# Kernel tuning notes

Hardware: AMD Instinct MI355X
Metric: run time of the kernel (lower is better)

Reference implementation:

```python
import jax, jax.numpy as jnp
import numpy as np

N_T, N_I = 4096, 4096
TEXT_DIM, IMAGE_DIM, HIDDEN_DIM = 1024, 1024, 1024


def setup_inputs() -> dict:
    key = jax.random.key(0)
    ks = jax.random.split(key, 8)
    s_t = 1.0 / np.sqrt(TEXT_DIM)
    s_i = 1.0 / np.sqrt(IMAGE_DIM)
    return {
        "text_features": jax.random.normal(ks[0], (N_T, TEXT_DIM), jnp.float32),
        "image_features": jax.random.normal(ks[1], (N_I, IMAGE_DIM), jnp.float32),
        # nn.Linear params: weight [out, in], bias [out]
        "w_text": jax.random.uniform(ks[2], (HIDDEN_DIM, TEXT_DIM), jnp.float32, -s_t, s_t),
        "b_text": jax.random.uniform(ks[3], (HIDDEN_DIM,), jnp.float32, -s_t, s_t),
        "w_image": jax.random.uniform(ks[4], (HIDDEN_DIM, IMAGE_DIM), jnp.float32, -s_i, s_i),
        "b_image": jax.random.uniform(ks[5], (HIDDEN_DIM,), jnp.float32, -s_i, s_i),
        "scale_TI": jnp.ones((1,), jnp.float32),
        "scale_IT": jnp.ones((1,), jnp.float32),
    }


def reference(text_features, image_features, w_text, b_text, w_image, b_image, scale_TI, scale_IT):
    # linear projections to shared hidden space
    t = text_features @ w_text.T + b_text      # [N_t, H]
    i = image_features @ w_image.T + b_image   # [N_i, H]
    inv_sqrt_h = 1.0 / jnp.sqrt(jnp.asarray(HIDDEN_DIM, t.dtype))
    # text -> image attention: softmax over image axis, scaled post-softmax
    logits_TI = (t @ i.T) * inv_sqrt_h               # [N_t, N_i]
    attn_TI = jax.nn.softmax(logits_TI, axis=-1) * scale_TI
    # image -> text attention
    attn_IT = jax.nn.softmax(logits_TI.T, axis=-1) * scale_IT  # [N_i, N_t]
    text_attention_on_image = attn_TI @ image_features  # [N_t, image_dim]
    image_attention_on_text = attn_IT @ text_features   # [N_i, text_dim]
    return (text_attention_on_image, image_attention_on_text)
```

## Files before the change

kernel.cpp:

```cpp
#include <hip/hip_runtime.h>


typedef __bf16 bf16x8 __attribute__((ext_vector_type(8)));
typedef float f32x4 __attribute__((ext_vector_type(4)));

#define N_T 4096
#define N_I 4096
#define DIM 1024
#define TSS 136

#define AT_SLOT 24576
#define AT_LDS_BYTES (3 * AT_SLOT * 2)

__device__ __forceinline__ unsigned short f2bf(float f) {
    unsigned int u = __float_as_uint(f);
    u += 0x7fffu + ((u >> 16) & 1u);
    return (unsigned short)(u >> 16);
}

__device__ __forceinline__ void async_cp16(const unsigned short* g, unsigned short* l) {
    __builtin_amdgcn_global_load_lds(
        (const __attribute__((address_space(1))) unsigned int*)g,
        (__attribute__((address_space(3))) unsigned int*)l, 16, 0, 0);
}

__device__ __forceinline__ void stage_async(const unsigned short* __restrict__ src,
                                            int ld, int row0, int k0,
                                            unsigned short* lds, int t) {
    int r = t >> 2, c = (t & 3) << 3;
    const unsigned short* g = src + (size_t)(row0 + r) * ld + k0 + c;
    async_cp16(g, lds + r * 32 + c);
    async_cp16(g + (size_t)64 * ld, lds + (64 + r) * 32 + c);
}

__device__ __forceinline__ void stage_async64(const unsigned short* __restrict__ src,
                                              int ld, int row0, int k0,
                                              unsigned short* lds, int t) {
    int r = t >> 2, c = (t & 3) << 3;
    async_cp16(src + (size_t)(row0 + r) * ld + k0 + c, lds + r * 32 + c);
}

__device__ __forceinline__ void mfma_step(const unsigned short* As,
                                          const unsigned short* Bs, f32x4 acc[4][4],
                                          int wrow, int wcol, int lane16, int quad) {
    bf16x8 a[4], b[4];
#pragma unroll
    for (int i = 0; i < 4; ++i) {
        a[i] = *(const bf16x8*)&As[(wrow + i * 16 + lane16) * 32 + quad * 8];
        b[i] = *(const bf16x8*)&Bs[(wcol + i * 16 + lane16) * 32 + quad * 8];
    }
#pragma unroll
    for (int i = 0; i < 4; ++i)
#pragma unroll
        for (int j = 0; j < 4; ++j)
            acc[i][j] = __builtin_amdgcn_mfma_f32_16x16x32_bf16(a[i], b[j], acc[i][j], 0, 0, 0);
}

__device__ __forceinline__ void mfma_step42(const unsigned short* As,
                                            const unsigned short* Bs, f32x4 acc[4][2],
                                            int wrow, int wcol, int lane16, int quad) {
    bf16x8 a[4], b[2];
#pragma unroll
    for (int i = 0; i < 4; ++i)
        a[i] = *(const bf16x8*)&As[(wrow + i * 16 + lane16) * 32 + quad * 8];
#pragma unroll
    for (int j = 0; j < 2; ++j)
        b[j] = *(const bf16x8*)&Bs[(wcol + j * 16 + lane16) * 32 + quad * 8];
#pragma unroll
    for (int i = 0; i < 4; ++i)
#pragma unroll
        for (int j = 0; j < 2; ++j)
            acc[i][j] = __builtin_amdgcn_mfma_f32_16x16x32_bf16(a[i], b[j], acc[i][j], 0, 0, 0);
}

__device__ __forceinline__ void tile_store(const unsigned short* sm,
                                           unsigned short* __restrict__ g, int ld,
                                           int row0, int col0, int tid) {
    int r = tid >> 1, h = (tid & 1) << 6;
    const unsigned short* src = sm + r * TSS + h;
    unsigned short* dst = g + (size_t)(row0 + r) * ld + col0 + h;
#pragma unroll
    for (int v = 0; v < 8; ++v)
        *(uint4*)(dst + v * 8) = *(const uint4*)(src + v * 8);
}

__global__ void __launch_bounds__(256)
cvt_all(const float* __restrict__ im, const float* __restrict__ tx,
        const float* __restrict__ wt, const float* __restrict__ wi,
        unsigned short* __restrict__ imb, unsigned short* __restrict__ txb,
        unsigned short* __restrict__ imgT, unsigned short* __restrict__ textT,
        unsigned short* __restrict__ wtb, unsigned short* __restrict__ wib,
        float* __restrict__ lTI) {
    int t = threadIdx.x;
    if (blockIdx.z == 2) {
        int lin = blockIdx.y * 64 + blockIdx.x;
        if (lin < 4) {
            *(f32x4*)&lTI[(lin * 256 + t) * 8] = (f32x4){0.f, 0.f, 0.f, 0.f};
            *(f32x4*)&lTI[(lin * 256 + t) * 8 + 4] = (f32x4){0.f, 0.f, 0.f, 0.f};
        }
        size_t i = (size_t)(lin * 256 + t) * 8;
        const float* s;
        unsigned short* d;
        size_t off;
        if (i < 1048576) { s = wt; d = wtb; off = i; }
        else             { s = wi; d = wib; off = i - 1048576; }
        float4 f0 = *(const float4*)(s + off);
        float4 f1 = *(const float4*)(s + off + 4);
        uint4 o;
        o.x = (unsigned int)f2bf(f0.x) | ((unsigned int)f2bf(f0.y) << 16);
        o.y = (unsigned int)f2bf(f0.z) | ((unsigned int)f2bf(f0.w) << 16);
        o.z = (unsigned int)f2bf(f1.x) | ((unsigned int)f2bf(f1.y) << 16);
        o.w = (unsigned int)f2bf(f1.z) | ((unsigned int)f2bf(f1.w) << 16);
        *(uint4*)(d + off) = o;
        return;
    }
    const float* in = blockIdx.z ? tx : im;
    unsigned short* nb = blockIdx.z ? txb : imb;
    unsigned short* tr = blockIdx.z ? textT : imgT;
    __shared__ float tile[64][65];
    int row0 = blockIdx.x * 64, col0 = blockIdx.y * 64;
    int r = t >> 2, c = (t & 3) << 4;
    {
        const float* p = in + (size_t)(row0 + r) * DIM + col0 + c;
        float4 f0 = *(const float4*)(p);
        float4 f1 = *(const float4*)(p + 4);
        float4 f2 = *(const float4*)(p + 8);
        float4 f3 = *(const float4*)(p + 12);
        *(float4*)&tile[r][c] = f0;
        *(float4*)&tile[r][c + 4] = f1;
        *(float4*)&tile[r][c + 8] = f2;
        *(float4*)&tile[r][c + 12] = f3;
        uint4 o0, o1;
        o0.x = (unsigned int)f2bf(f0.x) | ((unsigned int)f2bf(f0.y) << 16);
        o0.y = (unsigned int)f2bf(f0.z) | ((unsigned int)f2bf(f0.w) << 16);
        o0.z = (unsigned int)f2bf(f1.x) | ((unsigned int)f2bf(f1.y) << 16);
        o0.w = (unsigned int)f2bf(f1.z) | ((unsigned int)f2bf(f1.w) << 16);
        o1.x = (unsigned int)f2bf(f2.x) | ((unsigned int)f2bf(f2.y) << 16);
        o1.y = (unsigned int)f2bf(f2.z) | ((unsigned int)f2bf(f2.w) << 16);
        o1.z = (unsigned int)f2bf(f3.x) | ((unsigned int)f2bf(f3.y) << 16);
        o1.w = (unsigned int)f2bf(f3.z) | ((unsigned int)f2bf(f3.w) << 16);
        unsigned short* q = nb + (size_t)(row0 + r) * DIM + col0 + c;
        *(uint4*)q = o0;
        *(uint4*)(q + 8) = o1;
    }
    __syncthreads();
    {
        unsigned short v[16];
#pragma unroll
        for (int u = 0; u < 16; ++u) v[u] = f2bf(tile[c + u][r]);
        unsigned short* q = tr + (size_t)(col0 + r) * N_T + row0 + c;
        *(uint4*)q = *(uint4*)&v[0];
        *(uint4*)(q + 8) = *(uint4*)&v[8];
    }
}

__global__ void __launch_bounds__(256, 4)
gemm_proj2(const unsigned short* __restrict__ Atx, const unsigned short* __restrict__ Wtx,
           const float* __restrict__ btx, unsigned short* __restrict__ Ctx,
           const unsigned short* __restrict__ Aim, const unsigned short* __restrict__ Wim,
           const float* __restrict__ bim, unsigned short* __restrict__ Cim) {
    __shared__ unsigned short As[2][128 * 32];
    __shared__ unsigned short Bs[2][64 * 32];
    int z = blockIdx.z;
    const unsigned short* A = z ? Aim : Atx;
    const unsigned short* W = z ? Wim : Wtx;
    const float* bias = z ? bim : btx;
    unsigned short* C = z ? Cim : Ctx;
    int tid = threadIdx.x;
    int m0 = blockIdx.x * 128, n0 = blockIdx.y * 64;
    int lane = tid & 63, wave = tid >> 6;
    int lane16 = lane & 15, quad = lane >> 4;
    int wrow = (wave >> 1) * 64, wcol = (wave & 1) * 32;
    f32x4 acc[4][2];
    {
        f32x4 zz = {0.f, 0.f, 0.f, 0.f};
        for (int i = 0; i < 4; ++i)
            for (int j = 0; j < 2; ++j) acc[i][j] = zz;
    }
    for (int k0 = 0; k0 < DIM; k0 += 64) {
        stage_async(A, DIM, m0, k0, As[0], tid);
        stage_async64(W, DIM, n0, k0, Bs[0], tid);
        stage_async(A, DIM, m0, k0 + 32, As[1], tid);
        stage_async64(W, DIM, n0, k0 + 32, Bs[1], tid);
        __syncthreads();
        mfma_step42(As[0], Bs[0], acc, wrow, wcol, lane16, quad);
        mfma_step42(As[1], Bs[1], acc, wrow, wcol, lane16, quad);
        __syncthreads();
    }
#pragma unroll
    for (int j = 0; j < 2; ++j) {
        int col = n0 + wcol + j * 16 + lane16;
        float bv = bias[col];
#pragma unroll
        for (int i = 0; i < 4; ++i) {
            int rowb = m0 + wrow + i * 16 + quad * 4;
#pragma unroll
            for (int r = 0; r < 4; ++r)
                C[(size_t)(rowb + r) * DIM + col] = f2bf(acc[i][j][r] + bv);
        }
    }
}

__global__ void __launch_bounds__(256, 4)
gemm_logits_exp(const unsigned short* __restrict__ Tb,
                const unsigned short* __restrict__ Ib,
                unsigned short* __restrict__ P, unsigned short* __restrict__ PT,
                float* __restrict__ lT, float* __restrict__ lI) {
    __shared__ unsigned short smem[128 * TSS];
    unsigned short* As0 = smem;
    unsigned short* Bs0 = smem + 4096;
    unsigned short* As1 = smem + 8192;
    unsigned short* Bs1 = smem + 12288;
    float* lred = (float*)(smem + 16384);
    float* cred = lred + 128;
    int tid = threadIdx.x;
    int m0 = blockIdx.x * 128, n0 = blockIdx.y * 128;
    int lane = tid & 63, wave = tid >> 6;
    int lane16 = lane & 15, quad = lane >> 4;
    int wrow = (wave >> 1) * 64, wcol = (wave & 1) * 64;
    f32x4 acc[4][4];
    {
        f32x4 z = {0.f, 0.f, 0.f, 0.f};
        for (int i = 0; i < 4; ++i)
            for (int j = 0; j < 4; ++j) acc[i][j] = z;
    }
    for (int k0 = 0; k0 < DIM; k0 += 64) {
        stage_async(Tb, DIM, m0, k0, As0, tid);
        stage_async(Ib, DIM, n0, k0, Bs0, tid);
        stage_async(Tb, DIM, m0, k0 + 32, As1, tid);
        stage_async(Ib, DIM, n0, k0 + 32, Bs1, tid);
        __syncthreads();
        mfma_step(As0, Bs0, acc, wrow, wcol, lane16, quad);
        mfma_step(As1, Bs1, acc, wrow, wcol, lane16, quad);
        __syncthreads();
    }
#pragma unroll
    for (int i = 0; i < 4; ++i)
#pragma unroll
        for (int j = 0; j < 4; ++j)
#pragma unroll
            for (int r = 0; r < 4; ++r)
                acc[i][j][r] = __expf(acc[i][j][r] * 0.03125f);
    float rs[4][4];
#pragma unroll
    for (int i = 0; i < 4; ++i)
#pragma unroll
        for (int r = 0; r < 4; ++r) {
            float s = acc[i][0][r] + acc[i][1][r] + acc[i][2][r] + acc[i][3][r];
            s += __shfl_xor(s, 1); s += __shfl_xor(s, 2);
            s += __shfl_xor(s, 4); s += __shfl_xor(s, 8);
            rs[i][r] = s;
        }
    float cs[4];
#pragma unroll
    for (int j = 0; j < 4; ++j) {
        float s = 0.f;
#pragma unroll
        for (int i = 0; i < 4; ++i)
#pragma unroll
            for (int r = 0; r < 4; ++r) s += acc[i][j][r];
        s += __shfl_xor(s, 16); s += __shfl_xor(s, 32);
        cs[j] = s;
    }
    if (wave & 1) {
        if (lane16 == 0)
#pragma unroll
            for (int i = 0; i < 4; ++i)
#pragma unroll
                for (int r = 0; r < 4; ++r)
                    lred[wrow + i * 16 + quad * 4 + r] = rs[i][r];
    }
    if (wave >> 1) {
        if (quad == 0)
#pragma unroll
            for (int j = 0; j < 4; ++j)
                cred[wcol + j * 16 + lane16] = cs[j];
    }
    __syncthreads();
    if (!(wave & 1) && lane16 == 0) {
#pragma unroll
        for (int i = 0; i < 4; ++i)
#pragma unroll
            for (int r = 0; r < 4; ++r) {
                int row = wrow + i * 16 + quad * 4 + r;
                atomicAdd(&lT[m0 + row], rs[i][r] + lred[row]);
            }
    }
    if (!(wave >> 1) && quad == 0) {
#pragma unroll
        for (int j = 0; j < 4; ++j) {
            int col = wcol + j * 16 + lane16;
            atomicAdd(&lI[n0 + col], cs[j] + cred[col]);
        }
    }
    __syncthreads();
#pragma unroll
    for (int i = 0; i < 4; ++i)
#pragma unroll
        for (int j = 0; j < 4; ++j)
#pragma unroll
            for (int r = 0; r < 4; ++r)
                smem[(wrow + i * 16 + quad * 4 + r) * TSS + wcol + j * 16 + lane16] =
                    f2bf(acc[i][j][r]);
    __syncthreads();
    tile_store(smem, P, N_I, m0, n0, tid);
    __syncthreads();
#pragma unroll
    for (int i = 0; i < 4; ++i)
#pragma unroll
        for (int j = 0; j < 4; ++j) {
            unsigned int lo = (unsigned int)f2bf(acc[i][j][0]) |
                              ((unsigned int)f2bf(acc[i][j][1]) << 16);
            unsigned int hi = (unsigned int)f2bf(acc[i][j][2]) |
                              ((unsigned int)f2bf(acc[i][j][3]) << 16);
            uint2 v; v.x = lo; v.y = hi;
            *(uint2*)&smem[(wcol + j * 16 + lane16) * TSS + wrow + i * 16 + quad * 4] = v;
        }
    __syncthreads();
    tile_store(smem, PT, N_T, n0, m0, tid);
}


__device__ __forceinline__ void at_stageA_half(const unsigned short* __restrict__ g,
                                               int row0, int k0, unsigned short* lds,
                                               int t, int h) {
#pragma unroll
    for (int u = 0; u < 2; ++u) {
        int c = t + (h * 2 + u) * 512;
        int r = c >> 3;
        int kq = (c & 7) ^ (r & 7);
        async_cp16(g + (size_t)(row0 + r) * 4096 + k0 + (kq << 3), lds + c * 8);
    }
}

__device__ __forceinline__ void at_stageB_half(const unsigned short* __restrict__ g,
                                               int row0, int k0, unsigned short* lds,
                                               int t, int h) {
    int c = t + h * 512;
    int r = c >> 3;
    int kq = (c & 7) ^ (r & 7);
    async_cp16(g + (size_t)(row0 + r) * 4096 + k0 + (kq << 3), lds + c * 8);
}

__device__ __forceinline__ void at_stageA(const unsigned short* __restrict__ g,
                                          int row0, int k0, unsigned short* lds, int t) {
    at_stageA_half(g, row0, k0, lds, t, 0);
    at_stageA_half(g, row0, k0, lds, t, 1);
}
__device__ __forceinline__ void at_stageB(const unsigned short* __restrict__ g,
                                          int row0, int k0, unsigned short* lds, int t) {
    at_stageB_half(g, row0, k0, lds, t, 0);
    at_stageB_half(g, row0, k0, lds, t, 1);
}

template <int DO_STAGE>
__device__ __forceinline__ void at_sub(const unsigned short* cp,
                                       const unsigned short* __restrict__ A,
                                       const unsigned short* __restrict__ Bt,
                                       int m0, int n0, int kst, unsigned short* nsl,
                                       int t, f32x4 acc[4][4],
                                       int wrow, int wcol, int lane16, int quad, int ks) {
    const unsigned short* As = cp;
    const unsigned short* Bs = cp + 16384;
    bf16x8 a[4], b[4];
    int sw = (((ks << 2) | quad) ^ (lane16 & 7)) << 3;
#pragma unroll
    for (int i = 0; i < 4; ++i)
        a[i] = *(const bf16x8*)&As[(wrow + i * 16 + lane16) * 64 + sw];
#pragma unroll
    for (int j = 0; j < 4; ++j)
        b[j] = *(const bf16x8*)&Bs[(wcol + j * 16 + lane16) * 64 + sw];
    if (DO_STAGE) {
        at_stageA_half(A, m0, kst, nsl, t, ks);
        at_stageB_half(Bt, n0, kst, nsl + 16384, t, ks);
    }
    __builtin_amdgcn_s_setprio(1);
#pragma unroll
    for (int i = 0; i < 4; ++i)
#pragma unroll
        for (int j = 0; j < 4; ++j)
            acc[i][j] = __builtin_amdgcn_mfma_f32_16x16x32_bf16(a[i], b[j], acc[i][j], 0, 0, 0);
    __builtin_amdgcn_s_setprio(0);
}

__global__ void __launch_bounds__(512)
gemm_attn3(const unsigned short* __restrict__ P, const unsigned short* __restrict__ imgT,
           const float* __restrict__ lT, const float* __restrict__ sTI,
           float* __restrict__ out0,
           const unsigned short* __restrict__ PT, const unsigned short* __restrict__ textT,
           const float* __restrict__ lI, const float* __restrict__ sIT,
           float* __restrict__ out1) {
    extern __shared__ unsigned short sm[];
    int which = blockIdx.z;
    const unsigned short* A = which ? PT : P;
    const unsigned short* Bt = which ? textT : imgT;
    const float* l = which ? lI : lT;
    const float* sp = which ? sIT : sTI;
    float* out = which ? out1 : out0;

    int tid = threadIdx.x;
    int m0 = blockIdx.x * 256, n0 = blockIdx.y * 128;
    int lane = tid & 63, wave = tid >> 6;
    int lane16 = lane & 15, quad = lane >> 4;
    int wrow = (wave >> 1) * 64, wcol = (wave & 1) * 64;
    f32x4 acc[4][4];
    {
        f32x4 z = {0.f, 0.f, 0.f, 0.f};
        for (int i = 0; i < 4; ++i)
            for (int j = 0; j < 4; ++j) acc[i][j] = z;
    }

    at_stageA(A, m0, 0, sm, tid);
    at_stageB(Bt, n0, 0, sm + 16384, tid);
    at_stageA(A, m0, 64, sm + AT_SLOT, tid);
    at_stageB(Bt, n0, 64, sm + AT_SLOT + 16384, tid);
    asm volatile("s_waitcnt vmcnt(6)" ::: "memory");
    __builtin_amdgcn_s_barrier();

    int cur = 0;
    for (int s = 0; s < 62; ++s) {
        int ns = cur + 2; if (ns >= 3) ns -= 3;
        unsigned short* nsl = sm + ns * AT_SLOT;
        const unsigned short* cp = sm + cur * AT_SLOT;
        int kst = (s + 2) * 64;
        at_sub<1>(cp, A, Bt, m0, n0, kst, nsl, tid, acc, wrow, wcol, lane16, quad, 0);
        asm volatile("" ::: "memory");
        __builtin_amdgcn_s_barrier();
        asm volatile("" ::: "memory");
        at_sub<1>(cp, A, Bt, m0, n0, kst, nsl, tid, acc, wrow, wcol, lane16, quad, 1);
        asm volatile("s_waitcnt vmcnt(6) lgkmcnt(0)" ::: "memory");
        __builtin_amdgcn_s_barrier();
        cur += 1; if (cur >= 3) cur -= 3;
    }
    {
        const unsigned short* cp = sm + cur * AT_SLOT;
        at_sub<0>(cp, A, Bt, m0, n0, 0, nullptr, tid, acc, wrow, wcol, lane16, quad, 0);
        asm volatile("" ::: "memory");
        __builtin_amdgcn_s_barrier();
        asm volatile("" ::: "memory");
        at_sub<0>(cp, A, Bt, m0, n0, 0, nullptr, tid, acc, wrow, wcol, lane16, quad, 1);
        asm volatile("s_waitcnt vmcnt(0) lgkmcnt(0)" ::: "memory");
        __builtin_amdgcn_s_barrier();
        cur += 1; if (cur >= 3) cur -= 3;
    }
    {
        const unsigned short* cp = sm + cur * AT_SLOT;
        at_sub<0>(cp, A, Bt, m0, n0, 0, nullptr, tid, acc, wrow, wcol, lane16, quad, 0);
        at_sub<0>(cp, A, Bt, m0, n0, 0, nullptr, tid, acc, wrow, wcol, lane16, quad, 1);
    }

    float sc = sp[0];
#pragma unroll
    for (int i = 0; i < 4; ++i) {
        int rowb = m0 + wrow + i * 16 + quad * 4;
        float fac[4];
#pragma unroll
        for (int r = 0; r < 4; ++r) fac[r] = sc / l[rowb + r];
#pragma unroll
        for (int j = 0; j < 4; ++j) {
            int col = n0 + wcol + j * 16 + lane16;
#pragma unroll
            for (int r = 0; r < 4; ++r)
                out[(size_t)(rowb + r) * DIM + col] = acc[i][j][r] * fac[r];
        }
    }
}

extern "C" void kernel_launch(void* const* d_in, const int* in_sizes, int n_in,
                              void* d_out, int out_size, void* d_ws, size_t ws_size,
                              hipStream_t stream) {
    const float* text = (const float*)d_in[0];
    const float* image = (const float*)d_in[1];
    const float* w_text = (const float*)d_in[2];
    const float* b_text = (const float*)d_in[3];
    const float* w_image = (const float*)d_in[4];
    const float* b_image = (const float*)d_in[5];
    const float* scale_TI = (const float*)d_in[6];
    const float* scale_IT = (const float*)d_in[7];
    float* out0 = (float*)d_out;
    float* out1 = out0 + (size_t)N_T * DIM;

    char* ws = (char*)d_ws;
    unsigned short* text_bf = (unsigned short*)(ws);
    unsigned short* image_bf = (unsigned short*)(ws + (8ull << 20));
    unsigned short* wt_bf = (unsigned short*)(ws + (16ull << 20));
    unsigned short* wi_bf = (unsigned short*)(ws + (18ull << 20));
    unsigned short* P = (unsigned short*)(ws);
    unsigned short* imgT = (unsigned short*)(ws + (32ull << 20));
    unsigned short* textT = (unsigned short*)(ws + (40ull << 20));
    unsigned short* t_bf = (unsigned short*)(ws + (48ull << 20));
    unsigned short* i_bf = (unsigned short*)(ws + (56ull << 20));
    unsigned short* PT = (unsigned short*)(ws + (64ull << 20));
    float* lT = (float*)(ws + (96ull << 20));
    float* lI = (float*)(ws + (96ull << 20) + 16384);

    static bool lds_set = false;
    if (!lds_set) {
        hipFuncSetAttribute((const void*)gemm_attn3,
                            hipFuncAttributeMaxDynamicSharedMemorySize, AT_LDS_BYTES);
        lds_set = true;
    }

    cvt_all<<<dim3(N_T / 64, DIM / 64, 3), 256, 0, stream>>>(
        image, text, w_text, w_image, image_bf, text_bf, imgT, textT,
        wt_bf, wi_bf, lT);

    gemm_proj2<<<dim3(N_T / 128, DIM / 64, 2), 256, 0, stream>>>(
        text_bf, wt_bf, b_text, t_bf, image_bf, wi_bf, b_image, i_bf);

    gemm_logits_exp<<<dim3(N_T / 128, N_I / 128), 256, 0, stream>>>(t_bf, i_bf, P, PT, lT, lI);

    gemm_attn3<<<dim3(N_T / 256, DIM / 128, 2), 512, AT_LDS_BYTES, stream>>>(
        P, imgT, lT, scale_TI, out0, PT, textT, lI, scale_IT, out1);
}
```

Baseline: 246.1 us.

## Port logits GEMM to 256x128 tiles with triple-buffered swizzled async pipeline

The logits/exp GEMM now uses the same 512-thread, triple-buffered, XOR-swizzled async LDS pipeline as the attention GEMM, with a 256x128 tile in place of 128x128. Staging helpers are templated on leading dimension so both kernels can share them. The aim is to overlap global loads with MFMA work and reduce LDS bank conflicts and sync stalls. Column sums are now reduced across four wave bands, and the transposed tile store uses a wider padded layout. In exchange, dynamic LDS use grows and there are fewer blocks in flight.

```diff
diff --git a/kernel.cpp b/kernel.cpp
--- a/kernel.cpp
+++ b/kernel.cpp
@@ -8,6 +8,7 @@
 #define N_I 4096
 #define DIM 1024
 #define TSS 136
+#define PTS 264
 
 #define AT_SLOT 24576
 #define AT_LDS_BYTES (3 * AT_SLOT * 2)
@@ -40,22 +41,6 @@
     async_cp16(src + (size_t)(row0 + r) * ld + k0 + c, lds + r * 32 + c);
 }
 
-__device__ __forceinline__ void mfma_step(const unsigned short* As,
-                                          const unsigned short* Bs, f32x4 acc[4][4],
-                                          int wrow, int wcol, int lane16, int quad) {
-    bf16x8 a[4], b[4];
-#pragma unroll
-    for (int i = 0; i < 4; ++i) {
-        a[i] = *(const bf16x8*)&As[(wrow + i * 16 + lane16) * 32 + quad * 8];
-        b[i] = *(const bf16x8*)&Bs[(wcol + i * 16 + lane16) * 32 + quad * 8];
-    }
-#pragma unroll
-    for (int i = 0; i < 4; ++i)
-#pragma unroll
-        for (int j = 0; j < 4; ++j)
-            acc[i][j] = __builtin_amdgcn_mfma_f32_16x16x32_bf16(a[i], b[j], acc[i][j], 0, 0, 0);
-}
-
 __device__ __forceinline__ void mfma_step42(const unsigned short* As,
                                             const unsigned short* Bs, f32x4 acc[4][2],
                                             int wrow, int wcol, int lane16, int quad) {
@@ -73,11 +58,89 @@
             acc[i][j] = __builtin_amdgcn_mfma_f32_16x16x32_bf16(a[i], b[j], acc[i][j], 0, 0, 0);
 }
 
-__device__ __forceinline__ void tile_store(const unsigned short* sm,
-                                           unsigned short* __restrict__ g, int ld,
-                                           int row0, int col0, int tid) {
+
+template <int LD>
+__device__ __forceinline__ void at_stageA_half(const unsigned short* __restrict__ g,
+                                               int row0, int k0, unsigned short* lds,
+                                               int t, int h) {
+#pragma unroll
+    for (int u = 0; u < 2; ++u) {
+        int c = t + (h * 2 + u) * 512;
+        int r = c >> 3;
+        int kq = (c & 7) ^ (r & 7);
+        async_cp16(g + (size_t)(row0 + r) * LD + k0 + (kq << 3), lds + c * 8);
+    }
+}
+
+template <int LD>
+__device__ __forceinline__ void at_stageB_half(const unsigned short* __restrict__ g,
+                                               int row0, int k0, unsigned short* lds,
+                                               int t, int h) {
+    int c = t + h * 512;
+    int r = c >> 3;
+    int kq = (c & 7) ^ (r & 7);
+    async_cp16(g + (size_t)(row0 + r) * LD + k0 + (kq << 3), lds + c * 8);
+}
+
+template <int LD>
+__device__ __forceinline__ void at_stageA(const unsigned short* __restrict__ g,
+                                          int row0, int k0, unsigned short* lds, int t) {
+    at_stageA_half<LD>(g, row0, k0, lds, t, 0);
+    at_stageA_half<LD>(g, row0, k0, lds, t, 1);
+}
+template <int LD>
+__device__ __forceinline__ void at_stageB(const unsigned short* __restrict__ g,
+                                          int row0, int k0, unsigned short* lds, int t) {
+    at_stageB_half<LD>(g, row0, k0, lds, t, 0);
+    at_stageB_half<LD>(g, row0, k0, lds, t, 1);
+}
+
+template <int LD, int DO_STAGE>
+__device__ __forceinline__ void at_sub(const unsigned short* cp,
+                                       const unsigned short* __restrict__ A,
+                                       const unsigned short* __restrict__ Bt,
+                                       int m0, int n0, int kst, unsigned short* nsl,
+                                       int t, f32x4 acc[4][4],
+                                       int wrow, int wcol, int lane16, int quad, int ks) {
+    const unsigned short* As = cp;
+    const unsigned short* Bs = cp + 16384;
+    bf16x8 a[4], b[4];
+    int sw = (((ks << 2) | quad) ^ (lane16 & 7)) << 3;
+#pragma unroll
+    for (int i = 0; i < 4; ++i)
+        a[i] = *(const bf16x8*)&As[(wrow + i * 16 + lane16) * 64 + sw];
+#pragma unroll
+    for (int j = 0; j < 4; ++j)
+        b[j] = *(const bf16x8*)&Bs[(wcol + j * 16 + lane16) * 64 + sw];
+    if (DO_STAGE) {
+        at_stageA_half<LD>(A, m0, kst, nsl, t, ks);
+        at_stageB_half<LD>(Bt, n0, kst, nsl + 16384, t, ks);
+    }
+    __builtin_amdgcn_s_setprio(1);
+#pragma unroll
+    for (int i = 0; i < 4; ++i)
+#pragma unroll
+        for (int j = 0; j < 4; ++j)
+            acc[i][j] = __builtin_amdgcn_mfma_f32_16x16x32_bf16(a[i], b[j], acc[i][j], 0, 0, 0);
+    __builtin_amdgcn_s_setprio(0);
+}
+
+__device__ __forceinline__ void tile_store256(const unsigned short* smp,
+                                              unsigned short* __restrict__ g, int ld,
+                                              int row0, int col0, int tid) {
     int r = tid >> 1, h = (tid & 1) << 6;
-    const unsigned short* src = sm + r * TSS + h;
+    const unsigned short* src = smp + r * TSS + h;
+    unsigned short* dst = g + (size_t)(row0 + r) * ld + col0 + h;
+#pragma unroll
+    for (int v = 0; v < 8; ++v)
+        *(uint4*)(dst + v * 8) = *(const uint4*)(src + v * 8);
+}
+
+__device__ __forceinline__ void tile_store128x256(const unsigned short* smp,
+                                                  unsigned short* __restrict__ g, int ld,
+                                                  int row0, int col0, int tid) {
+    int r = tid >> 2, h = (tid & 3) << 6;
+    const unsigned short* src = smp + r * PTS + h;
     unsigned short* dst = g + (size_t)(row0 + r) * ld + col0 + h;
 #pragma unroll
     for (int v = 0; v < 8; ++v)
@@ -201,20 +264,14 @@
     }
 }
 
-__global__ void __launch_bounds__(256, 4)
+__global__ void __launch_bounds__(512)
 gemm_logits_exp(const unsigned short* __restrict__ Tb,
                 const unsigned short* __restrict__ Ib,
                 unsigned short* __restrict__ P, unsigned short* __restrict__ PT,
                 float* __restrict__ lT, float* __restrict__ lI) {
-    __shared__ unsigned short smem[128 * TSS];
-    unsigned short* As0 = smem;
-    unsigned short* Bs0 = smem + 4096;
-    unsigned short* As1 = smem + 8192;
-    unsigned short* Bs1 = smem + 12288;
-    float* lred = (float*)(smem + 16384);
-    float* cred = lred + 128;
+    extern __shared__ unsigned short sm[];
     int tid = threadIdx.x;
-    int m0 = blockIdx.x * 128, n0 = blockIdx.y * 128;
+    int m0 = blockIdx.x * 256, n0 = blockIdx.y * 128;
     int lane = tid & 63, wave = tid >> 6;
     int lane16 = lane & 15, quad = lane >> 4;
     int wrow = (wave >> 1) * 64, wcol = (wave & 1) * 64;
@@ -224,16 +281,46 @@
         for (int i = 0; i < 4; ++i)
             for (int j = 0; j < 4; ++j) acc[i][j] = z;
     }
-    for (int k0 = 0; k0 < DIM; k0 += 64) {
-        stage_async(Tb, DIM, m0, k0, As0, tid);
-        stage_async(Ib, DIM, n0, k0, Bs0, tid);
-        stage_async(Tb, DIM, m0, k0 + 32, As1, tid);
-        stage_async(Ib, DIM, n0, k0 + 32, Bs1, tid);
-        __syncthreads();
-        mfma_step(As0, Bs0, acc, wrow, wcol, lane16, quad);
-        mfma_step(As1, Bs1, acc, wrow, wcol, lane16, quad);
-        __syncthreads();
-    }
+
+    at_stageA<DIM>(Tb, m0, 0, sm, tid);
+    at_stageB<DIM>(Ib, n0, 0, sm + 16384, tid);
+    at_stageA<DIM>(Tb, m0, 64, sm + AT_SLOT, tid);
+    at_stageB<DIM>(Ib, n0, 64, sm + AT_SLOT + 16384, tid);
+    asm volatile("s_waitcnt vmcnt(6)" ::: "memory");
+    __builtin_amdgcn_s_barrier();
+
+    int cur = 0;
+    for (int s = 0; s < 14; ++s) {
+        int ns = cur + 2; if (ns >= 3) ns -= 3;
+        unsigned short* nsl = sm + ns * AT_SLOT;
+        const unsigned short* cp = sm + cur * AT_SLOT;
+        int kst = (s + 2) * 64;
+        at_sub<DIM, 1>(cp, Tb, Ib, m0, n0, kst, nsl, tid, acc, wrow, wcol, lane16, quad, 0);
+        asm volatile("" ::: "memory");
+        __builtin_amdgcn_s_barrier();
+        asm volatile("" ::: "memory");
+        at_sub<DIM, 1>(cp, Tb, Ib, m0, n0, kst, nsl, tid, acc, wrow, wcol, lane16, quad, 1);
+        asm volatile("s_waitcnt vmcnt(6) lgkmcnt(0)" ::: "memory");
+        __builtin_amdgcn_s_barrier();
+        cur += 1; if (cur >= 3) cur -= 3;
+    }
+    {
+        const unsigned short* cp = sm + cur * AT_SLOT;
+        at_sub<DIM, 0>(cp, Tb, Ib, m0, n0, 0, nullptr, tid, acc, wrow, wcol, lane16, quad, 0);
+        asm volatile("" ::: "memory");
+        __builtin_amdgcn_s_barrier();
+        asm volatile("" ::: "memory");
+        at_sub<DIM, 0>(cp, Tb, Ib, m0, n0, 0, nullptr, tid, acc, wrow, wcol, lane16, quad, 1);
+        asm volatile("s_waitcnt vmcnt(0) lgkmcnt(0)" ::: "memory");
+        __builtin_amdgcn_s_barrier();
+        cur += 1; if (cur >= 3) cur -= 3;
+    }
+    {
+        const unsigned short* cp = sm + cur * AT_SLOT;
+        at_sub<DIM, 0>(cp, Tb, Ib, m0, n0, 0, nullptr, tid, acc, wrow, wcol, lane16, quad, 0);
+        at_sub<DIM, 0>(cp, Tb, Ib, m0, n0, 0, nullptr, tid, acc, wrow, wcol, lane16, quad, 1);
+    }
+
 #pragma unroll
     for (int i = 0; i < 4; ++i)
 #pragma unroll
@@ -262,6 +349,10 @@
         s += __shfl_xor(s, 16); s += __shfl_xor(s, 32);
         cs[j] = s;
     }
+    float* lred = (float*)(sm + 35840);
+    float* cred = lred + 256;
+    int band = wave >> 1;
+    __syncthreads();
     if (wave & 1) {
         if (lane16 == 0)
 #pragma unroll
@@ -270,12 +361,20 @@
                 for (int r = 0; r < 4; ++r)
                     lred[wrow + i * 16 + quad * 4 + r] = rs[i][r];
     }
-    if (wave >> 1) {
+    if (band) {
         if (quad == 0)
 #pragma unroll
             for (int j = 0; j < 4; ++j)
-                cred[wcol + j * 16 + lane16] = cs[j];
-    }
+                cred[(band - 1) * 128 + wcol + j * 16 + lane16] = cs[j];
+    }
+#pragma unroll
+    for (int i = 0; i < 4; ++i)
+#pragma unroll
+        for (int j = 0; j < 4; ++j)
+#pragma unroll
+            for (int r = 0; r < 4; ++r)
+                sm[(wrow + i * 16 + quad * 4 + r) * TSS + wcol + j * 16 + lane16] =
+                    f2bf(acc[i][j][r]);
     __syncthreads();
     if (!(wave & 1) && lane16 == 0) {
 #pragma unroll
@@ -286,24 +385,14 @@
                 atomicAdd(&lT[m0 + row], rs[i][r] + lred[row]);
             }
     }
-    if (!(wave >> 1) && quad == 0) {
+    if (!band && quad == 0) {
 #pragma unroll
         for (int j = 0; j < 4; ++j) {
-            int col = wcol + j * 16 + lane16;
-            atomicAdd(&lI[n0 + col], cs[j] + cred[col]);
+            int c = wcol + j * 16 + lane16;
+            atomicAdd(&lI[n0 + c], cs[j] + cred[c] + cred[128 + c] + cred[256 + c]);
         }
     }
-    __syncthreads();
-#pragma unroll
-    for (int i = 0; i < 4; ++i)
-#pragma unroll
-        for (int j = 0; j < 4; ++j)
-#pragma unroll
-            for (int r = 0; r < 4; ++r)
-                smem[(wrow + i * 16 + quad * 4 + r) * TSS + wcol + j * 16 + lane16] =
-                    f2bf(acc[i][j][r]);
-    __syncthreads();
-    tile_store(smem, P, N_I, m0, n0, tid);
+    tile_store256(sm, P, N_I, m0, n0, tid);
     __syncthreads();
 #pragma unroll
     for (int i = 0; i < 4; ++i)
@@ -314,73 +403,10 @@
             unsigned int hi = (unsigned int)f2bf(acc[i][j][2]) |
                               ((unsigned int)f2bf(acc[i][j][3]) << 16);
             uint2 v; v.x = lo; v.y = hi;
-            *(uint2*)&smem[(wcol + j * 16 + lane16) * TSS + wrow + i * 16 + quad * 4] = v;
+            *(uint2*)&sm[(wcol + j * 16 + lane16) * PTS + wrow + i * 16 + quad * 4] = v;
         }
     __syncthreads();
-    tile_store(smem, PT, N_T, n0, m0, tid);
-}
-
-
-__device__ __forceinline__ void at_stageA_half(const unsigned short* __restrict__ g,
-                                               int row0, int k0, unsigned short* lds,
-                                               int t, int h) {
-#pragma unroll
-    for (int u = 0; u < 2; ++u) {
-        int c = t + (h * 2 + u) * 512;
-        int r = c >> 3;
-        int kq = (c & 7) ^ (r & 7);
-        async_cp16(g + (size_t)(row0 + r) * 4096 + k0 + (kq << 3), lds + c * 8);
-    }
-}
-
-__device__ __forceinline__ void at_stageB_half(const unsigned short* __restrict__ g,
-                                               int row0, int k0, unsigned short* lds,
-                                               int t, int h) {
-    int c = t + h * 512;
-    int r = c >> 3;
-    int kq = (c & 7) ^ (r & 7);
-    async_cp16(g + (size_t)(row0 + r) * 4096 + k0 + (kq << 3), lds + c * 8);
-}
-
-__device__ __forceinline__ void at_stageA(const unsigned short* __restrict__ g,
-                                          int row0, int k0, unsigned short* lds, int t) {
-    at_stageA_half(g, row0, k0, lds, t, 0);
-    at_stageA_half(g, row0, k0, lds, t, 1);
-}
-__device__ __forceinline__ void at_stageB(const unsigned short* __restrict__ g,
-                                          int row0, int k0, unsigned short* lds, int t) {
-    at_stageB_half(g, row0, k0, lds, t, 0);
-    at_stageB_half(g, row0, k0, lds, t, 1);
-}
-
-template <int DO_STAGE>
-__device__ __forceinline__ void at_sub(const unsigned short* cp,
-                                       const unsigned short* __restrict__ A,
-                                       const unsigned short* __restrict__ Bt,
-                                       int m0, int n0, int kst, unsigned short* nsl,
-                                       int t, f32x4 acc[4][4],
-                                       int wrow, int wcol, int lane16, int quad, int ks) {
-    const unsigned short* As = cp;
-    const unsigned short* Bs = cp + 16384;
-    bf16x8 a[4], b[4];
-    int sw = (((ks << 2) | quad) ^ (lane16 & 7)) << 3;
-#pragma unroll
-    for (int i = 0; i < 4; ++i)
-        a[i] = *(const bf16x8*)&As[(wrow + i * 16 + lane16) * 64 + sw];
-#pragma unroll
-    for (int j = 0; j < 4; ++j)
-        b[j] = *(const bf16x8*)&Bs[(wcol + j * 16 + lane16) * 64 + sw];
-    if (DO_STAGE) {
-        at_stageA_half(A, m0, kst, nsl, t, ks);
-        at_stageB_half(Bt, n0, kst, nsl + 16384, t, ks);
-    }
-    __builtin_amdgcn_s_setprio(1);
-#pragma unroll
-    for (int i = 0; i < 4; ++i)
-#pragma unroll
-        for (int j = 0; j < 4; ++j)
-            acc[i][j] = __builtin_amdgcn_mfma_f32_16x16x32_bf16(a[i], b[j], acc[i][j], 0, 0, 0);
-    __builtin_amdgcn_s_setprio(0);
+    tile_store128x256(sm, PT, N_T, n0, m0, tid);
 }
 
 __global__ void __launch_bounds__(512)
@@ -410,10 +436,10 @@
             for (int j = 0; j < 4; ++j) acc[i][j] = z;
     }
 
-    at_stageA(A, m0, 0, sm, tid);
-    at_stageB(Bt, n0, 0, sm + 16384, tid);
-    at_stageA(A, m0, 64, sm + AT_SLOT, tid);
-    at_stageB(Bt, n0, 64, sm + AT_SLOT + 16384, tid);
+    at_stageA<4096>(A, m0, 0, sm, tid);
+    at_stageB<4096>(Bt, n0, 0, sm + 16384, tid);
+    at_stageA<4096>(A, m0, 64, sm + AT_SLOT, tid);
+    at_stageB<4096>(Bt, n0, 64, sm + AT_SLOT + 16384, tid);
     asm volatile("s_waitcnt vmcnt(6)" ::: "memory");
     __builtin_amdgcn_s_barrier();
 
@@ -423,30 +449,30 @@
         unsigned short* nsl = sm + ns * AT_SLOT;
         const unsigned short* cp = sm + cur * AT_SLOT;
         int kst = (s + 2) * 64;
-        at_sub<1>(cp, A, Bt, m0, n0, kst, nsl, tid, acc, wrow, wcol, lane16, quad, 0);
-        asm volatile("" ::: "memory");
-        __builtin_amdgcn_s_barrier();
-        asm volatile("" ::: "memory");
-        at_sub<1>(cp, A, Bt, m0, n0, kst, nsl, tid, acc, wrow, wcol, lane16, quad, 1);
+        at_sub<4096, 1>(cp, A, Bt, m0, n0, kst, nsl, tid, acc, wrow, wcol, lane16, quad, 0);
+        asm volatile("" ::: "memory");
+        __builtin_amdgcn_s_barrier();
+        asm volatile("" ::: "memory");
+        at_sub<4096, 1>(cp, A, Bt, m0, n0, kst, nsl, tid, acc, wrow, wcol, lane16, quad, 1);
         asm volatile("s_waitcnt vmcnt(6) lgkmcnt(0)" ::: "memory");
         __builtin_amdgcn_s_barrier();
         cur += 1; if (cur >= 3) cur -= 3;
     }
     {
         const unsigned short* cp = sm + cur * AT_SLOT;
-        at_sub<0>(cp, A, Bt, m0, n0, 0, nullptr, tid, acc, wrow, wcol, lane16, quad, 0);
-        asm volatile("" ::: "memory");
-        __builtin_amdgcn_s_barrier();
-        asm volatile("" ::: "memory");
-        at_sub<0>(cp, A, Bt, m0, n0, 0, nullptr, tid, acc, wrow, wcol, lane16, quad, 1);
+        at_sub<4096, 0>(cp, A, Bt, m0, n0, 0, nullptr, tid, acc, wrow, wcol, lane16, quad, 0);
+        asm volatile("" ::: "memory");
+        __builtin_amdgcn_s_barrier();
+        asm volatile("" ::: "memory");
+        at_sub<4096, 0>(cp, A, Bt, m0, n0, 0, nullptr, tid, acc, wrow, wcol, lane16, quad, 1);
         asm volatile("s_waitcnt vmcnt(0) lgkmcnt(0)" ::: "memory");
         __builtin_amdgcn_s_barrier();
         cur += 1; if (cur >= 3) cur -= 3;
     }
     {
         const unsigned short* cp = sm + cur * AT_SLOT;
-        at_sub<0>(cp, A, Bt, m0, n0, 0, nullptr, tid, acc, wrow, wcol, lane16, quad, 0);
-        at_sub<0>(cp, A, Bt, m0, n0, 0, nullptr, tid, acc, wrow, wcol, lane16, quad, 1);
+        at_sub<4096, 0>(cp, A, Bt, m0, n0, 0, nullptr, tid, acc, wrow, wcol, lane16, quad, 0);
+        at_sub<4096, 0>(cp, A, Bt, m0, n0, 0, nullptr, tid, acc, wrow, wcol, lane16, quad, 1);
     }
 
     float sc = sp[0];
@@ -498,6 +524,8 @@
     if (!lds_set) {
         hipFuncSetAttribute((const void*)gemm_attn3,
                             hipFuncAttributeMaxDynamicSharedMemorySize, AT_LDS_BYTES);
+        hipFuncSetAttribute((const void*)gemm_logits_exp,
+                            hipFuncAttributeMaxDynamicSharedMemorySize, AT_LDS_BYTES);
         lds_set = true;
     }
 
@@ -508,7 +536,8 @@
     gemm_proj2<<<dim3(N_T / 128, DIM / 64, 2), 256, 0, stream>>>(
         text_bf, wt_bf, b_text, t_bf, image_bf, wi_bf, b_image, i_bf);
 
-    gemm_logits_exp<<<dim3(N_T / 128, N_I / 128), 256, 0, stream>>>(t_bf, i_bf, P, PT, lT, lI);
+    gemm_logits_exp<<<dim3(N_T / 256, N_I / 128), 512, AT_LDS_BYTES, stream>>>(
+        t_bf, i_bf, P, PT, lT, lI);
 
     gemm_attn3<<<dim3(N_T / 256, DIM / 128, 2), 512, AT_LDS_BYTES, stream>>>(
         P, imgT, lT, scale_TI, out0, PT, textT, lI, scale_IT, out1);
```

Result: slower. 252.5 us (+2.6%).

## Load A fragments directly from global into registers, stage only B in LDS

Applied to the files above, without the earlier changes.

The attention GEMM stops staging the A operand (the softmax probability matrix) through LDS. Each wave now loads its A fragments straight from global memory into registers, double-buffered one k-tile ahead, while B keeps the 3-slot async LDS pipeline. This cuts LDS footprint from 144KB to 48KB, which may allow more blocks per CU, and removes the LDS write and read traffic for A. The cost is that A rows are no longer shared between the two waves with the same wrow, so global and L2 load traffic for A doubles. It also needs more registers and exposes global load latency directly to the MFMA loop.

```diff
diff --git a/kernel.cpp b/kernel.cpp
--- a/kernel.cpp
+++ b/kernel.cpp
@@ -9,8 +9,7 @@
 #define DIM 1024
 #define TSS 136
 
-#define AT_SLOT 24576
-#define AT_LDS_BYTES (3 * AT_SLOT * 2)
+#define BT_SLOT 8192
 
 __device__ __forceinline__ unsigned short f2bf(float f) {
     unsigned int u = __float_as_uint(f);
@@ -321,18 +320,6 @@
 }
 
 
-__device__ __forceinline__ void at_stageA_half(const unsigned short* __restrict__ g,
-                                               int row0, int k0, unsigned short* lds,
-                                               int t, int h) {
-#pragma unroll
-    for (int u = 0; u < 2; ++u) {
-        int c = t + (h * 2 + u) * 512;
-        int r = c >> 3;
-        int kq = (c & 7) ^ (r & 7);
-        async_cp16(g + (size_t)(row0 + r) * 4096 + k0 + (kq << 3), lds + c * 8);
-    }
-}
-
 __device__ __forceinline__ void at_stageB_half(const unsigned short* __restrict__ g,
                                                int row0, int k0, unsigned short* lds,
                                                int t, int h) {
@@ -341,56 +328,70 @@
     int kq = (c & 7) ^ (r & 7);
     async_cp16(g + (size_t)(row0 + r) * 4096 + k0 + (kq << 3), lds + c * 8);
 }
-
-__device__ __forceinline__ void at_stageA(const unsigned short* __restrict__ g,
-                                          int row0, int k0, unsigned short* lds, int t) {
-    at_stageA_half(g, row0, k0, lds, t, 0);
-    at_stageA_half(g, row0, k0, lds, t, 1);
-}
 __device__ __forceinline__ void at_stageB(const unsigned short* __restrict__ g,
                                           int row0, int k0, unsigned short* lds, int t) {
     at_stageB_half(g, row0, k0, lds, t, 0);
     at_stageB_half(g, row0, k0, lds, t, 1);
 }
 
+__device__ __forceinline__ void load_afrags(const unsigned short* Arow, int k0,
+                                            bf16x8 a[8]) {
+#pragma unroll
+    for (int i = 0; i < 4; ++i)
+#pragma unroll
+        for (int ks = 0; ks < 2; ++ks)
+            a[i * 2 + ks] = *(const bf16x8*)(Arow + (size_t)i * 16 * 4096 + k0 + ks * 32);
+}
+
 template <int DO_STAGE>
-__device__ __forceinline__ void at_sub(const unsigned short* cp,
-                                       const unsigned short* __restrict__ A,
-                                       const unsigned short* __restrict__ Bt,
-                                       int m0, int n0, int kst, unsigned short* nsl,
-                                       int t, f32x4 acc[4][4],
-                                       int wrow, int wcol, int lane16, int quad, int ks) {
-    const unsigned short* As = cp;
-    const unsigned short* Bs = cp + 16384;
-    bf16x8 a[4], b[4];
+__device__ __forceinline__ void at4_sub(const unsigned short* Bs, const bf16x8 a[8],
+                                        const unsigned short* __restrict__ Bt,
+                                        int n0, int kst, unsigned short* nsl,
+                                        int t, f32x4 acc[4][4],
+                                        int wcol, int lane16, int quad, int ks) {
+    bf16x8 b[4];
     int sw = (((ks << 2) | quad) ^ (lane16 & 7)) << 3;
-#pragma unroll
-    for (int i = 0; i < 4; ++i)
-        a[i] = *(const bf16x8*)&As[(wrow + i * 16 + lane16) * 64 + sw];
 #pragma unroll
     for (int j = 0; j < 4; ++j)
         b[j] = *(const bf16x8*)&Bs[(wcol + j * 16 + lane16) * 64 + sw];
-    if (DO_STAGE) {
-        at_stageA_half(A, m0, kst, nsl, t, ks);
-        at_stageB_half(Bt, n0, kst, nsl + 16384, t, ks);
-    }
+    if (DO_STAGE)
+        at_stageB_half(Bt, n0, kst, nsl, t, ks);
     __builtin_amdgcn_s_setprio(1);
 #pragma unroll
     for (int i = 0; i < 4; ++i)
 #pragma unroll
         for (int j = 0; j < 4; ++j)
-            acc[i][j] = __builtin_amdgcn_mfma_f32_16x16x32_bf16(a[i], b[j], acc[i][j], 0, 0, 0);
+            acc[i][j] = __builtin_amdgcn_mfma_f32_16x16x32_bf16(a[i * 2 + ks], b[j],
+                                                               acc[i][j], 0, 0, 0);
     __builtin_amdgcn_s_setprio(0);
 }
 
+__device__ __forceinline__ void at4_tile(const unsigned short* Bs, unsigned short* nsl,
+                                         const unsigned short* Arow,
+                                         const unsigned short* __restrict__ Bt,
+                                         int n0, int ka, int kb,
+                                         const bf16x8 aC[8], bf16x8 aN[8],
+                                         int t, f32x4 acc[4][4],
+                                         int wcol, int lane16, int quad) {
+    load_afrags(Arow, ka, aN);
+    __builtin_amdgcn_sched_barrier(0);
+    at4_sub<1>(Bs, aC, Bt, n0, kb, nsl, t, acc, wcol, lane16, quad, 0);
+    asm volatile("" ::: "memory");
+    __builtin_amdgcn_s_barrier();
+    asm volatile("" ::: "memory");
+    at4_sub<1>(Bs, aC, Bt, n0, kb, nsl, t, acc, wcol, lane16, quad, 1);
+    asm volatile("s_waitcnt vmcnt(2) lgkmcnt(0)" ::: "memory");
+    __builtin_amdgcn_s_barrier();
+}
+
 __global__ void __launch_bounds__(512)
-gemm_attn3(const unsigned short* __restrict__ P, const unsigned short* __restrict__ imgT,
+gemm_attn4(const unsigned short* __restrict__ P, const unsigned short* __restrict__ imgT,
            const float* __restrict__ lT, const float* __restrict__ sTI,
            float* __restrict__ out0,
            const unsigned short* __restrict__ PT, const unsigned short* __restrict__ textT,
            const float* __restrict__ lI, const float* __restrict__ sIT,
            float* __restrict__ out1) {
-    extern __shared__ unsigned short sm[];
+    __shared__ unsigned short Bsm[3 * BT_SLOT];
     int which = blockIdx.z;
     const unsigned short* A = which ? PT : P;
     const unsigned short* Bt = which ? textT : imgT;
@@ -403,50 +404,54 @@
     int lane = tid & 63, wave = tid >> 6;
     int lane16 = lane & 15, quad = lane >> 4;
     int wrow = (wave >> 1) * 64, wcol = (wave & 1) * 64;
+    const unsigned short* Arow = A + (size_t)(m0 + wrow + lane16) * 4096 + quad * 8;
     f32x4 acc[4][4];
     {
         f32x4 z = {0.f, 0.f, 0.f, 0.f};
         for (int i = 0; i < 4; ++i)
             for (int j = 0; j < 4; ++j) acc[i][j] = z;
     }
-
-    at_stageA(A, m0, 0, sm, tid);
-    at_stageB(Bt, n0, 0, sm + 16384, tid);
-    at_stageA(A, m0, 64, sm + AT_SLOT, tid);
-    at_stageB(Bt, n0, 64, sm + AT_SLOT + 16384, tid);
-    asm volatile("s_waitcnt vmcnt(6)" ::: "memory");
+    bf16x8 aA[8], aB[8];
+
+    at_stageB(Bt, n0, 0, Bsm, tid);
+    at_stageB(Bt, n0, 64, Bsm + BT_SLOT, tid);
+    load_afrags(Arow, 0, aA);
+    asm volatile("s_waitcnt vmcnt(10)" ::: "memory");
     __builtin_amdgcn_s_barrier();
 
     int cur = 0;
-    for (int s = 0; s < 62; ++s) {
-        int ns = cur + 2; if (ns >= 3) ns -= 3;
-        unsigned short* nsl = sm + ns * AT_SLOT;
-        const unsigned short* cp = sm + cur * AT_SLOT;
-        int kst = (s + 2) * 64;
-        at_sub<1>(cp, A, Bt, m0, n0, kst, nsl, tid, acc, wrow, wcol, lane16, quad, 0);
+    for (int s2 = 0; s2 < 31; ++s2) {
+        int s = s2 * 2;
+        {
+            int ns = cur + 2; if (ns >= 3) ns -= 3;
+            at4_tile(Bsm + cur * BT_SLOT, Bsm + ns * BT_SLOT, Arow, Bt, n0,
+                     (s + 1) * 64, (s + 2) * 64, aA, aB, tid, acc, wcol, lane16, quad);
+            cur += 1; if (cur >= 3) cur -= 3;
+        }
+        {
+            int ns = cur + 2; if (ns >= 3) ns -= 3;
+            at4_tile(Bsm + cur * BT_SLOT, Bsm + ns * BT_SLOT, Arow, Bt, n0,
+                     (s + 2) * 64, (s + 3) * 64, aB, aA, tid, acc, wcol, lane16, quad);
+            cur += 1; if (cur >= 3) cur -= 3;
+        }
+    }
+    {
+        const unsigned short* Bs = Bsm + cur * BT_SLOT;
+        load_afrags(Arow, 63 * 64, aB);
+        __builtin_amdgcn_sched_barrier(0);
+        at4_sub<0>(Bs, aA, nullptr, 0, 0, nullptr, tid, acc, wcol, lane16, quad, 0);
         asm volatile("" ::: "memory");
         __builtin_amdgcn_s_barrier();
         asm volatile("" ::: "memory");
-        at_sub<1>(cp, A, Bt, m0, n0, kst, nsl, tid, acc, wrow, wcol, lane16, quad, 1);
-        asm volatile("s_waitcnt vmcnt(6) lgkmcnt(0)" ::: "memory");
-        __builtin_amdgcn_s_barrier();
-        cur += 1; if (cur >= 3) cur -= 3;
-    }
-    {
-        const unsigned short* cp = sm + cur * AT_SLOT;
-        at_sub<0>(cp, A, Bt, m0, n0, 0, nullptr, tid, acc, wrow, wcol, lane16, quad, 0);
-        asm volatile("" ::: "memory");
-        __builtin_amdgcn_s_barrier();
-        asm volatile("" ::: "memory");
-        at_sub<0>(cp, A, Bt, m0, n0, 0, nullptr, tid, acc, wrow, wcol, lane16, quad, 1);
+        at4_sub<0>(Bs, aA, nullptr, 0, 0, nullptr, tid, acc, wcol, lane16, quad, 1);
         asm volatile("s_waitcnt vmcnt(0) lgkmcnt(0)" ::: "memory");
         __builtin_amdgcn_s_barrier();
         cur += 1; if (cur >= 3) cur -= 3;
     }
     {
-        const unsigned short* cp = sm + cur * AT_SLOT;
-        at_sub<0>(cp, A, Bt, m0, n0, 0, nullptr, tid, acc, wrow, wcol, lane16, quad, 0);
-        at_sub<0>(cp, A, Bt, m0, n0, 0, nullptr, tid, acc, wrow, wcol, lane16, quad, 1);
+        const unsigned short* Bs = Bsm + cur * BT_SLOT;
+        at4_sub<0>(Bs, aB, nullptr, 0, 0, nullptr, tid, acc, wcol, lane16, quad, 0);
+        at4_sub<0>(Bs, aB, nullptr, 0, 0, nullptr, tid, acc, wcol, lane16, quad, 1);
     }
 
     float sc = sp[0];
@@ -494,13 +499,6 @@
     float* lT = (float*)(ws + (96ull << 20));
     float* lI = (float*)(ws + (96ull << 20) + 16384);
 
-    static bool lds_set = false;
-    if (!lds_set) {
-        hipFuncSetAttribute((const void*)gemm_attn3,
-                            hipFuncAttributeMaxDynamicSharedMemorySize, AT_LDS_BYTES);
-        lds_set = true;
-    }
-
     cvt_all<<<dim3(N_T / 64, DIM / 64, 3), 256, 0, stream>>>(
         image, text, w_text, w_image, image_bf, text_bf, imgT, textT,
         wt_bf, wi_bf, lT);
@@ -510,6 +508,6 @@
 
     gemm_logits_exp<<<dim3(N_T / 128, N_I / 128), 256, 0, stream>>>(t_bf, i_bf, P, PT, lT, lI);
 
-    gemm_attn3<<<dim3(N_T / 256, DIM / 128, 2), 512, AT_LDS_BYTES, stream>>>(
+    gemm_attn4<<<dim3(N_T / 256, DIM / 128, 2), 512, 0, stream>>>(
         P, imgT, lT, scale_TI, out0, PT, textT, lI, scale_IT, out1);
 }
```

Result: slower. 334.9 us (+36.1%).
